# Kernel optimization log

Hardware: AMD Instinct MI355X
Metric: run time of the kernel (lower is better)

Reference implementation:

```python
import jax, jax.numpy as jnp
import numpy as np

DIM = 512
WH, WW = 8, 8
N = WH * WW
HEADS = 16
HEAD_DIM = DIM // HEADS
SCALE = HEAD_DIM ** -0.5
TABLE = (2 * WH - 1) * (2 * WW - 1)  # 225


def _relative_position_index(wh, ww):
    coords = np.stack(np.meshgrid(np.arange(wh), np.arange(ww), indexing='ij'))  # (2, wh, ww)
    flat = coords.reshape(2, -1)                       # (2, N)
    rel = flat[:, :, None] - flat[:, None, :]          # (2, N, N)
    rel = rel.transpose(1, 2, 0).astype(np.int64)      # (N, N, 2)
    rel[..., 0] += wh - 1
    rel[..., 1] += ww - 1
    rel[..., 0] *= 2 * ww - 1
    return rel.sum(-1)                                 # (N, N)

REL_IDX = _relative_position_index(WH, WW)


def setup_inputs() -> dict:
    key = jax.random.key(0)
    ks = jax.random.split(key, 10)
    B_ = 2048
    nW = 64
    x = jax.random.normal(ks[0], (B_, N, DIM), dtype=jnp.float32)
    y = jax.random.normal(ks[1], (B_, N, DIM), dtype=jnp.float32)
    mask = jnp.zeros((nW, N, N), dtype=jnp.float32)  # 0/-inf shift mask; zeros = no shift
    W_q = jax.random.normal(ks[2], (DIM, DIM), dtype=jnp.float32) * 0.02
    b_q = jnp.zeros((DIM,), dtype=jnp.float32)
    W_kv = jax.random.normal(ks[3], (DIM, 2 * DIM), dtype=jnp.float32) * 0.02
    b_kv = jnp.zeros((2 * DIM,), dtype=jnp.float32)
    W_proj = jax.random.normal(ks[4], (DIM, DIM), dtype=jnp.float32) * 0.02
    b_proj = jnp.zeros((DIM,), dtype=jnp.float32)
    bias_table = jax.random.normal(ks[5], (TABLE, HEADS), dtype=jnp.float32) * 0.02
    return {"x": x, "y": y, "mask": mask, "W_q": W_q, "b_q": b_q,
            "W_kv": W_kv, "b_kv": b_kv, "W_proj": W_proj, "b_proj": b_proj,
            "bias_table": bias_table}


def reference(x, y, mask, W_q, b_q, W_kv, b_kv, W_proj, b_proj, bias_table):
    B_, n, C = x.shape
    # projections
    q = (x @ W_q + b_q).reshape(B_, n, HEADS, HEAD_DIM).transpose(0, 2, 1, 3)       # (B_,H,N,hd)
    kv = (y @ W_kv + b_kv).reshape(B_, n, 2, HEADS, HEAD_DIM).transpose(2, 0, 3, 1, 4)
    k, v = kv[0], kv[1]                                                              # (B_,H,N,hd)
    q = q * SCALE
    attn = jnp.einsum('bhnd,bhmd->bhnm', q, k)                                       # (B_,H,N,N)
    # relative position bias gather: (N*N,) -> (N,N,H) -> (H,N,N)
    bias = bias_table[REL_IDX.reshape(-1)].reshape(n, n, HEADS).transpose(2, 0, 1)
    attn = attn + bias[None]
    nW = mask.shape[0]
    attn = attn.reshape(B_ // nW, nW, HEADS, n, n) + mask[None, :, None]
    attn = attn.reshape(B_, HEADS, n, n)
    attn = jax.nn.softmax(attn, axis=-1)
    out = jnp.einsum('bhnm,bhmd->bhnd', attn, v)                                     # (B_,H,N,hd)
    out = out.transpose(0, 2, 1, 3).reshape(B_, n, C)
    out = out @ W_proj + b_proj
    return out
```

## Files before the change

### kernel.cpp

```cpp
#include <hip/hip_runtime.h>
#include <stdint.h>

#define MROWS 131072
#define LOG2E 1.44269504088896340736f
#define QSCALE 0.17677669529663688110f

typedef _Float16 f16x8 __attribute__((ext_vector_type(8)));
typedef float f32x4 __attribute__((ext_vector_type(4)));
typedef unsigned short u16;
typedef u16 u16x4 __attribute__((ext_vector_type(4)));
typedef u16 u16x8 __attribute__((ext_vector_type(8)));

#define GLD16(gp, lp) __builtin_amdgcn_global_load_lds( \
    (const __attribute__((address_space(1))) void*)(gp), \
    (__attribute__((address_space(3))) void*)(lp), 16, 0, 0)

static __device__ __forceinline__ u16 f2h(float f) {
    _Float16 h = (_Float16)f;
    return __builtin_bit_cast(unsigned short, h);
}
static __device__ __forceinline__ float shflx(float v, int m) {
    return __shfl_xor(v, m, 64);
}
static __device__ __forceinline__ int swz4096(int bid) {
    return (bid & 7) * 512 + (bid >> 3);
}

__global__ void wt_f16(const float* __restrict__ W, int ldW, int colOff,
                       u16* __restrict__ WT, int K) {
    int idx = blockIdx.x * 256 + threadIdx.x;
    int n = idx / K, k = idx - n * K;
    WT[idx] = f2h(W[(size_t)k * ldW + colOff + n]);
}
__global__ void cmb_pre(const float* __restrict__ table, const float* __restrict__ mask,
                        float* __restrict__ cmb) {
    int wmod = blockIdx.x, h = blockIdx.y;
    float* outp = cmb + (((size_t)wmod * 16 + h) << 12);
    const float* mp = mask + ((size_t)wmod << 12);
    for (int e = threadIdx.x; e < 4096; e += 256) {
        int j = e >> 6, i = e & 63;
        int idx = ((i >> 3) - (j >> 3) + 7) * 15 + ((i & 7) - (j & 7) + 7);
        outp[e] = table[idx * 16 + h] + mp[i * 64 + j];
    }
}

__global__ __launch_bounds__(256, 4) void gemm_qk(
    const float* __restrict__ A, const u16* __restrict__ BT,
    const float* __restrict__ bias, u16* __restrict__ outp, float scale)
{
    __shared__ u16 As[128 * 32];
    __shared__ u16 Bs[128 * 32];
    const int tid = threadIdx.x;
    const int l = tid & 63, w = tid >> 6;
    const int al = l & 15, g = l >> 4;
    const int wr = w >> 1, wc = w & 1;
    const int wg = swz4096(blockIdx.x);
    const int n0 = (wg & 3) * 128, m0 = (wg >> 2) * 128;
    const int srow = tid >> 2, sc8 = (tid & 3) * 8;
    f32x4 acc[4][4] = {};

    for (int kk = 0; kk < 512; kk += 32) {
        #pragma unroll
        for (int r = 0; r < 2; ++r) {
            int row = r * 64 + srow;
            GLD16(BT + (size_t)(n0 + row) * 512 + kk + sc8, &Bs[row * 32 + sc8]);
            const float* ap = A + (size_t)(m0 + row) * 512 + kk + sc8;
            f32x4 v0 = *(const f32x4*)(ap);
            f32x4 v1 = *(const f32x4*)(ap + 4);
            u16x8 hv;
            hv[0]=f2h(v0[0]); hv[1]=f2h(v0[1]); hv[2]=f2h(v0[2]); hv[3]=f2h(v0[3]);
            hv[4]=f2h(v1[0]); hv[5]=f2h(v1[1]); hv[6]=f2h(v1[2]); hv[7]=f2h(v1[3]);
            *(u16x8*)&As[row * 32 + sc8] = hv;
        }
        __syncthreads();
        {
            f16x8 af[4], bfr[4];
            #pragma unroll
            for (int mt = 0; mt < 4; ++mt)
                af[mt] = *(const f16x8*)&As[(wr*64 + mt*16 + al) * 32 + g*8];
            #pragma unroll
            for (int nt = 0; nt < 4; ++nt)
                bfr[nt] = *(const f16x8*)&Bs[(wc*64 + nt*16 + al) * 32 + g*8];
            #pragma unroll
            for (int mt = 0; mt < 4; ++mt)
                #pragma unroll
                for (int nt = 0; nt < 4; ++nt)
                    acc[mt][nt] = __builtin_amdgcn_mfma_f32_16x16x32_f16(af[mt], bfr[nt], acc[mt][nt], 0, 0, 0);
        }
        __syncthreads();
    }
    #pragma unroll
    for (int nt = 0; nt < 4; ++nt) {
        int col = n0 + wc*64 + nt*16 + al;
        float bv = bias[col];
        #pragma unroll
        for (int mt = 0; mt < 4; ++mt)
            #pragma unroll
            for (int rg = 0; rg < 4; ++rg) {
                size_t row = (size_t)(m0 + wr*64 + mt*16 + g*4 + rg);
                outp[row * 512 + col] = f2h((acc[mt][nt][rg] + bv) * scale);
            }
    }
}

__global__ __launch_bounds__(256, 4) void gemm_v(
    const float* __restrict__ A, const u16* __restrict__ BT,
    const float* __restrict__ bias, u16* __restrict__ outp)
{
    __shared__ u16 As[128*32], Bs[128*32];
    const int tid = threadIdx.x;
    const int l = tid & 63, w = tid >> 6;
    const int al = l & 15, g = l >> 4;
    const int wr = w >> 1, wc = w & 1;
    const int wg = swz4096(blockIdx.x);
    const int n0 = (wg & 3) * 128, m0 = (wg >> 2) * 128;
    const int srow = tid >> 2, sc8 = (tid & 3) * 8;
    f32x4 acc[4][4] = {};

    for (int kk = 0; kk < 512; kk += 32) {
        #pragma unroll
        for (int r = 0; r < 2; ++r) {
            int row = r * 64 + srow;
            GLD16(BT + (size_t)(n0 + row) * 512 + kk + sc8, &Bs[row * 32 + sc8]);
            const float* ap = A + (size_t)(m0 + row) * 512 + kk + sc8;
            f32x4 v0 = *(const f32x4*)(ap);
            f32x4 v1 = *(const f32x4*)(ap + 4);
            u16x8 hv;
            hv[0]=f2h(v0[0]); hv[1]=f2h(v0[1]); hv[2]=f2h(v0[2]); hv[3]=f2h(v0[3]);
            hv[4]=f2h(v1[0]); hv[5]=f2h(v1[1]); hv[6]=f2h(v1[2]); hv[7]=f2h(v1[3]);
            *(u16x8*)&As[row * 32 + sc8] = hv;
        }
        __syncthreads();
        {
            f16x8 af[4], bfr[4];
            #pragma unroll
            for (int mt = 0; mt < 4; ++mt)
                af[mt] = *(const f16x8*)&As[(wr*64 + mt*16 + al) * 32 + g*8];
            #pragma unroll
            for (int nt = 0; nt < 4; ++nt)
                bfr[nt] = *(const f16x8*)&Bs[(wc*64 + nt*16 + al) * 32 + g*8];
            #pragma unroll
            for (int mt = 0; mt < 4; ++mt)
                #pragma unroll
                for (int nt = 0; nt < 4; ++nt)
                    acc[mt][nt] = __builtin_amdgcn_mfma_f32_16x16x32_f16(af[mt], bfr[nt], acc[mt][nt], 0, 0, 0);
        }
        __syncthreads();
    }
    #pragma unroll
    for (int nt = 0; nt < 4; ++nt) {
        int col = n0 + wc*64 + nt*16 + al;
        int hh_ = col >> 5, d = col & 31;
        float bv = bias[col];
        #pragma unroll
        for (int mt = 0; mt < 4; ++mt) {
            int row0 = m0 + wr*64 + mt*16 + g*4;
            int window = row0 >> 6, k0 = row0 & 63;
            size_t off = ((size_t)window << 15) + (hh_ << 11) + (d << 6) + k0;
            u16x4 hv;
            #pragma unroll
            for (int rg = 0; rg < 4; ++rg)
                hv[rg] = f2h(acc[mt][nt][rg] + bv);
            *(u16x4*)(outp + off) = hv;
        }
    }
}

__global__ __launch_bounds__(256, 4) void gemm_proj(
    const u16* __restrict__ A1, const u16* __restrict__ BT,
    const float* __restrict__ bias, float* __restrict__ outp)
{
    __shared__ u16 As[128*32], Bs[128*32];
    const int tid = threadIdx.x;
    const int l = tid & 63, w = tid >> 6;
    const int al = l & 15, g = l >> 4;
    const int wr = w >> 1, wc = w & 1;
    const int wg = swz4096(blockIdx.x);
    const int n0 = (wg & 3) * 128, m0 = (wg >> 2) * 128;
    const int srow = tid >> 2, sc8 = (tid & 3) * 8;
    f32x4 acc[4][4] = {};

    for (int kk = 0; kk < 512; kk += 32) {
        #pragma unroll
        for (int r = 0; r < 2; ++r) {
            int row = r * 64 + srow;
            size_t aoff = (size_t)(m0 + row) * 512 + kk + sc8;
            size_t boff = (size_t)(n0 + row) * 512 + kk + sc8;
            int loff = row * 32 + sc8;
            GLD16(A1 + aoff, &As[loff]);
            GLD16(BT + boff, &Bs[loff]);
        }
        __syncthreads();
        {
            f16x8 af[4], bfr[4];
            #pragma unroll
            for (int mt = 0; mt < 4; ++mt)
                af[mt] = *(const f16x8*)&As[(wr*64 + mt*16 + al) * 32 + g*8];
            #pragma unroll
            for (int nt = 0; nt < 4; ++nt)
                bfr[nt] = *(const f16x8*)&Bs[(wc*64 + nt*16 + al) * 32 + g*8];
            #pragma unroll
            for (int mt = 0; mt < 4; ++mt)
                #pragma unroll
                for (int nt = 0; nt < 4; ++nt)
                    acc[mt][nt] = __builtin_amdgcn_mfma_f32_16x16x32_f16(af[mt], bfr[nt], acc[mt][nt], 0, 0, 0);
        }
        __syncthreads();
    }
    #pragma unroll
    for (int nt = 0; nt < 4; ++nt) {
        int col = n0 + wc*64 + nt*16 + al;
        float bv = bias[col];
        #pragma unroll
        for (int mt = 0; mt < 4; ++mt)
            #pragma unroll
            for (int rg = 0; rg < 4; ++rg) {
                size_t row = (size_t)(m0 + wr*64 + mt*16 + g*4 + rg);
                outp[row * 512 + col] = acc[mt][nt][rg] + bv;
            }
    }
}

__global__ __launch_bounds__(256) void attn64(
    const u16* __restrict__ Q, const u16* __restrict__ Kb,
    const u16* __restrict__ Vth,
    const float* __restrict__ cmb,
    u16* __restrict__ Oout)
{
    __shared__ u16 Ph[4][64 * 72];
    const int bid = blockIdx.x;
    const int xcd = bid & 7, idx = bid >> 3;
    const int b = ((idx >> 3) << 6) | (xcd << 3) | (idx & 7);
    const int tid = threadIdx.x;
    const int l = tid & 63, w = tid >> 6;
    const int al = l & 15, g = l >> 4;
    const size_t rbase = (size_t)b * 64;
    const int h = blockIdx.y * 4 + w;
    const int co = h * 32;

    const u16* vth = Vth + ((size_t)b << 15) + (h << 11);
    f16x8 vhf[2][2];
    #pragma unroll
    for (int kt = 0; kt < 2; ++kt)
        #pragma unroll
        for (int dt = 0; dt < 2; ++dt) {
            int voff = ((dt*16 + al) << 6) + kt*32 + g*8;
            vhf[kt][dt] = *(const f16x8*)(vth + voff);
        }

    f16x8 qf[4], kf[4];
    #pragma unroll
    for (int t = 0; t < 4; ++t) {
        qf[t] = *(const f16x8*)(Q  + (rbase + t*16 + al) * 512 + co + g*8);
        kf[t] = *(const f16x8*)(Kb + (rbase + t*16 + al) * 512 + co + g*8);
    }
    f32x4 s[4][4] = {};
    #pragma unroll
    for (int mt = 0; mt < 4; ++mt)
        #pragma unroll
        for (int nt = 0; nt < 4; ++nt)
            s[mt][nt] = __builtin_amdgcn_mfma_f32_16x16x32_f16(qf[mt], kf[nt], s[mt][nt], 0, 0, 0);

    const float* cp = cmb + ((((size_t)(b & 63)) * 16 + h) << 12);
    #pragma unroll
    for (int mt = 0; mt < 4; ++mt)
        #pragma unroll
        for (int nt = 0; nt < 4; ++nt) {
            f32x4 c4 = *(const f32x4*)(cp + ((nt*16 + al) << 6) + mt*16 + g*4);
            #pragma unroll
            for (int rg = 0; rg < 4; ++rg) s[mt][nt][rg] += c4[rg];
        }

    f32x4 sm[4];
    #pragma unroll
    for (int mt = 0; mt < 4; ++mt) {
        f32x4 m4 = s[mt][0];
        #pragma unroll
        for (int nt = 1; nt < 4; ++nt)
            #pragma unroll
            for (int c = 0; c < 4; ++c) m4[c] = fmaxf(m4[c], s[mt][nt][c]);
        #pragma unroll
        for (int d = 1; d < 16; d <<= 1)
            #pragma unroll
            for (int c = 0; c < 4; ++c) m4[c] = fmaxf(m4[c], shflx(m4[c], d));
        #pragma unroll
        for (int nt = 0; nt < 4; ++nt)
            #pragma unroll
            for (int rg = 0; rg < 4; ++rg)
                s[mt][nt][rg] = exp2f((s[mt][nt][rg] - m4[rg]) * LOG2E);
        f32x4 s4 = s[mt][0];
        #pragma unroll
        for (int nt = 1; nt < 4; ++nt) s4 += s[mt][nt];
        #pragma unroll
        for (int d = 1; d < 16; d <<= 1)
            #pragma unroll
            for (int c = 0; c < 4; ++c) s4[c] += shflx(s4[c], d);
        sm[mt] = s4;
    }

    #pragma unroll
    for (int mt = 0; mt < 4; ++mt)
        #pragma unroll
        for (int nt = 0; nt < 4; ++nt)
            #pragma unroll
            for (int rg = 0; rg < 4; ++rg) {
                int off = (mt*16 + g*4 + rg) * 72 + nt*16 + al;
                Ph[w][off] = f2h(s[mt][nt][rg]);
            }

    #pragma unroll
    for (int mt = 0; mt < 4; ++mt) {
        f16x8 pah[2];
        #pragma unroll
        for (int kt = 0; kt < 2; ++kt)
            pah[kt] = *(const f16x8*)&Ph[w][(mt*16 + al) * 72 + kt*32 + g*8];
        f32x4 o[2] = {};
        #pragma unroll
        for (int dt = 0; dt < 2; ++dt)
            #pragma unroll
            for (int kt = 0; kt < 2; ++kt)
                o[dt] = __builtin_amdgcn_mfma_f32_16x16x32_f16(pah[kt], vhf[kt][dt], o[dt], 0, 0, 0);
        #pragma unroll
        for (int dt = 0; dt < 2; ++dt)
            #pragma unroll
            for (int rg = 0; rg < 4; ++rg) {
                float inv = __builtin_amdgcn_rcpf(sm[mt][rg]);
                float v = o[dt][rg] * inv;
                size_t off = (rbase + mt*16 + g*4 + rg) * 512 + co + dt*16 + al;
                Oout[off] = f2h(v);
            }
    }
}

extern "C" void kernel_launch(void* const* d_in, const int* in_sizes, int n_in,
                              void* d_out, int out_size, void* d_ws, size_t ws_size,
                              hipStream_t stream)
{
    const float* x      = (const float*)d_in[0];
    const float* y      = (const float*)d_in[1];
    const float* mask   = (const float*)d_in[2];
    const float* W_q    = (const float*)d_in[3];
    const float* b_q    = (const float*)d_in[4];
    const float* W_kv   = (const float*)d_in[5];
    const float* b_kv   = (const float*)d_in[6];
    const float* W_proj = (const float*)d_in[7];
    const float* b_proj = (const float*)d_in[8];
    const float* table  = (const float*)d_in[9];

    char* ws = (char*)d_ws;
    const size_t SEG = (size_t)MROWS * 512 * sizeof(u16);
    u16* Qs     = (u16*)(ws);
    u16* Ks     = (u16*)(ws + SEG);
    u16* Vth    = (u16*)(ws + 2 * SEG);
    u16* wqT    = (u16*)(ws + 3 * SEG);
    u16* wkvKT  = wqT    + 512 * 512;
    u16* wkvVT  = wkvKT  + 512 * 512;
    u16* wprT   = wkvVT  + 512 * 512;
    float* cmb  = (float*)(wprT + 512 * 512);

    wt_f16<<<1024, 256, 0, stream>>>(W_q, 512, 0, wqT, 512);
    wt_f16<<<1024, 256, 0, stream>>>(W_kv, 1024, 0, wkvKT, 512);
    wt_f16<<<1024, 256, 0, stream>>>(W_kv, 1024, 512, wkvVT, 512);
    wt_f16<<<1024, 256, 0, stream>>>(W_proj, 512, 0, wprT, 512);
    cmb_pre<<<dim3(64, 16), 256, 0, stream>>>(table, mask, cmb);

    gemm_qk<<<4096, 256, 0, stream>>>(x, wqT, b_q, Qs, QSCALE);
    gemm_qk<<<4096, 256, 0, stream>>>(y, wkvKT, b_kv, Ks, 1.0f);
    gemm_v<<<4096, 256, 0, stream>>>(y, wkvVT, b_kv + 512, Vth);
    attn64<<<dim3(2048, 4), 256, 0, stream>>>(Qs, Ks, Vth, cmb, Qs);
    gemm_proj<<<4096, 256, 0, stream>>>(Qs, wprT, b_proj, (float*)d_out);
}
```

Before: 782.7 us.

## Double-buffer LDS tiles in projection GEMMs to overlap loads with MFMA

Converts the three projection GEMM kernels to a double-buffered shared-memory pipeline. The next K-slice's global loads (register prefetch for fp32 A, direct-to-LDS loads for B) are issued before the current slice's MFMAs, and one of the two barriers per iteration is removed. This is meant to hide global memory latency behind compute. It doubles LDS per block to 32KB, which may limit occupancy under launch_bounds(256,4), and the single-barrier scheme relies on the direct-to-LDS loads having completed when the barrier is reached.

```diff
diff --git a/kernel.cpp b/kernel.cpp
--- a/kernel.cpp
+++ b/kernel.cpp
@@ -48,8 +48,8 @@
     const float* __restrict__ A, const u16* __restrict__ BT,
     const float* __restrict__ bias, u16* __restrict__ outp, float scale)
 {
-    __shared__ u16 As[128 * 32];
-    __shared__ u16 Bs[128 * 32];
+    __shared__ u16 As[2][128 * 32];
+    __shared__ u16 Bs[2][128 * 32];
     const int tid = threadIdx.x;
     const int l = tid & 63, w = tid >> 6;
     const int al = l & 15, g = l >> 4;
@@ -57,37 +57,56 @@
     const int wg = swz4096(blockIdx.x);
     const int n0 = (wg & 3) * 128, m0 = (wg >> 2) * 128;
     const int srow = tid >> 2, sc8 = (tid & 3) * 8;
+    const float* asrc0 = A  + (size_t)(m0 + srow) * 512 + sc8;
+    const float* asrc1 = A  + (size_t)(m0 + 64 + srow) * 512 + sc8;
+    const u16*   bsrc0 = BT + (size_t)(n0 + srow) * 512 + sc8;
+    const u16*   bsrc1 = BT + (size_t)(n0 + 64 + srow) * 512 + sc8;
+    const int lo0 = srow * 32 + sc8, lo1 = (64 + srow) * 32 + sc8;
     f32x4 acc[4][4] = {};
 
-    for (int kk = 0; kk < 512; kk += 32) {
-        #pragma unroll
-        for (int r = 0; r < 2; ++r) {
-            int row = r * 64 + srow;
-            GLD16(BT + (size_t)(n0 + row) * 512 + kk + sc8, &Bs[row * 32 + sc8]);
-            const float* ap = A + (size_t)(m0 + row) * 512 + kk + sc8;
-            f32x4 v0 = *(const f32x4*)(ap);
-            f32x4 v1 = *(const f32x4*)(ap + 4);
-            u16x8 hv;
-            hv[0]=f2h(v0[0]); hv[1]=f2h(v0[1]); hv[2]=f2h(v0[2]); hv[3]=f2h(v0[3]);
-            hv[4]=f2h(v1[0]); hv[5]=f2h(v1[1]); hv[6]=f2h(v1[2]); hv[7]=f2h(v1[3]);
-            *(u16x8*)&As[row * 32 + sc8] = hv;
+    f32x4 a00 = *(const f32x4*)(asrc0);
+    f32x4 a01 = *(const f32x4*)(asrc0 + 4);
+    f32x4 a10 = *(const f32x4*)(asrc1);
+    f32x4 a11 = *(const f32x4*)(asrc1 + 4);
+    GLD16(bsrc0, &Bs[0][lo0]);
+    GLD16(bsrc1, &Bs[0][lo1]);
+
+    #pragma unroll 2
+    for (int it = 0; it < 16; ++it) {
+        const int cur = it & 1, nxt = cur ^ 1;
+        {
+            u16x8 h0, h1;
+            h0[0]=f2h(a00[0]); h0[1]=f2h(a00[1]); h0[2]=f2h(a00[2]); h0[3]=f2h(a00[3]);
+            h0[4]=f2h(a01[0]); h0[5]=f2h(a01[1]); h0[6]=f2h(a01[2]); h0[7]=f2h(a01[3]);
+            h1[0]=f2h(a10[0]); h1[1]=f2h(a10[1]); h1[2]=f2h(a10[2]); h1[3]=f2h(a10[3]);
+            h1[4]=f2h(a11[0]); h1[5]=f2h(a11[1]); h1[6]=f2h(a11[2]); h1[7]=f2h(a11[3]);
+            *(u16x8*)&As[cur][lo0] = h0;
+            *(u16x8*)&As[cur][lo1] = h1;
         }
         __syncthreads();
+        if (it < 15) {
+            const int kn = (it + 1) * 32;
+            a00 = *(const f32x4*)(asrc0 + kn);
+            a01 = *(const f32x4*)(asrc0 + kn + 4);
+            a10 = *(const f32x4*)(asrc1 + kn);
+            a11 = *(const f32x4*)(asrc1 + kn + 4);
+            GLD16(bsrc0 + kn, &Bs[nxt][lo0]);
+            GLD16(bsrc1 + kn, &Bs[nxt][lo1]);
+        }
         {
             f16x8 af[4], bfr[4];
             #pragma unroll
             for (int mt = 0; mt < 4; ++mt)
-                af[mt] = *(const f16x8*)&As[(wr*64 + mt*16 + al) * 32 + g*8];
+                af[mt] = *(const f16x8*)&As[cur][(wr*64 + mt*16 + al) * 32 + g*8];
             #pragma unroll
             for (int nt = 0; nt < 4; ++nt)
-                bfr[nt] = *(const f16x8*)&Bs[(wc*64 + nt*16 + al) * 32 + g*8];
+                bfr[nt] = *(const f16x8*)&Bs[cur][(wc*64 + nt*16 + al) * 32 + g*8];
             #pragma unroll
             for (int mt = 0; mt < 4; ++mt)
                 #pragma unroll
                 for (int nt = 0; nt < 4; ++nt)
                     acc[mt][nt] = __builtin_amdgcn_mfma_f32_16x16x32_f16(af[mt], bfr[nt], acc[mt][nt], 0, 0, 0);
         }
-        __syncthreads();
     }
     #pragma unroll
     for (int nt = 0; nt < 4; ++nt) {
@@ -107,7 +126,8 @@
     const float* __restrict__ A, const u16* __restrict__ BT,
     const float* __restrict__ bias, u16* __restrict__ outp)
 {
-    __shared__ u16 As[128*32], Bs[128*32];
+    __shared__ u16 As[2][128 * 32];
+    __shared__ u16 Bs[2][128 * 32];
     const int tid = threadIdx.x;
     const int l = tid & 63, w = tid >> 6;
     const int al = l & 15, g = l >> 4;
@@ -115,37 +135,56 @@
     const int wg = swz4096(blockIdx.x);
     const int n0 = (wg & 3) * 128, m0 = (wg >> 2) * 128;
     const int srow = tid >> 2, sc8 = (tid & 3) * 8;
+    const float* asrc0 = A  + (size_t)(m0 + srow) * 512 + sc8;
+    const float* asrc1 = A  + (size_t)(m0 + 64 + srow) * 512 + sc8;
+    const u16*   bsrc0 = BT + (size_t)(n0 + srow) * 512 + sc8;
+    const u16*   bsrc1 = BT + (size_t)(n0 + 64 + srow) * 512 + sc8;
+    const int lo0 = srow * 32 + sc8, lo1 = (64 + srow) * 32 + sc8;
     f32x4 acc[4][4] = {};
 
-    for (int kk = 0; kk < 512; kk += 32) {
-        #pragma unroll
-        for (int r = 0; r < 2; ++r) {
-            int row = r * 64 + srow;
-            GLD16(BT + (size_t)(n0 + row) * 512 + kk + sc8, &Bs[row * 32 + sc8]);
-            const float* ap = A + (size_t)(m0 + row) * 512 + kk + sc8;
-            f32x4 v0 = *(const f32x4*)(ap);
-            f32x4 v1 = *(const f32x4*)(ap + 4);
-            u16x8 hv;
-            hv[0]=f2h(v0[0]); hv[1]=f2h(v0[1]); hv[2]=f2h(v0[2]); hv[3]=f2h(v0[3]);
-            hv[4]=f2h(v1[0]); hv[5]=f2h(v1[1]); hv[6]=f2h(v1[2]); hv[7]=f2h(v1[3]);
-            *(u16x8*)&As[row * 32 + sc8] = hv;
+    f32x4 a00 = *(const f32x4*)(asrc0);
+    f32x4 a01 = *(const f32x4*)(asrc0 + 4);
+    f32x4 a10 = *(const f32x4*)(asrc1);
+    f32x4 a11 = *(const f32x4*)(asrc1 + 4);
+    GLD16(bsrc0, &Bs[0][lo0]);
+    GLD16(bsrc1, &Bs[0][lo1]);
+
+    #pragma unroll 2
+    for (int it = 0; it < 16; ++it) {
+        const int cur = it & 1, nxt = cur ^ 1;
+        {
+            u16x8 h0, h1;
+            h0[0]=f2h(a00[0]); h0[1]=f2h(a00[1]); h0[2]=f2h(a00[2]); h0[3]=f2h(a00[3]);
+            h0[4]=f2h(a01[0]); h0[5]=f2h(a01[1]); h0[6]=f2h(a01[2]); h0[7]=f2h(a01[3]);
+            h1[0]=f2h(a10[0]); h1[1]=f2h(a10[1]); h1[2]=f2h(a10[2]); h1[3]=f2h(a10[3]);
+            h1[4]=f2h(a11[0]); h1[5]=f2h(a11[1]); h1[6]=f2h(a11[2]); h1[7]=f2h(a11[3]);
+            *(u16x8*)&As[cur][lo0] = h0;
+            *(u16x8*)&As[cur][lo1] = h1;
         }
         __syncthreads();
+        if (it < 15) {
+            const int kn = (it + 1) * 32;
+            a00 = *(const f32x4*)(asrc0 + kn);
+            a01 = *(const f32x4*)(asrc0 + kn + 4);
+            a10 = *(const f32x4*)(asrc1 + kn);
+            a11 = *(const f32x4*)(asrc1 + kn + 4);
+            GLD16(bsrc0 + kn, &Bs[nxt][lo0]);
+            GLD16(bsrc1 + kn, &Bs[nxt][lo1]);
+        }
         {
             f16x8 af[4], bfr[4];
             #pragma unroll
             for (int mt = 0; mt < 4; ++mt)
-                af[mt] = *(const f16x8*)&As[(wr*64 + mt*16 + al) * 32 + g*8];
+                af[mt] = *(const f16x8*)&As[cur][(wr*64 + mt*16 + al) * 32 + g*8];
             #pragma unroll
             for (int nt = 0; nt < 4; ++nt)
-                bfr[nt] = *(const f16x8*)&Bs[(wc*64 + nt*16 + al) * 32 + g*8];
+                bfr[nt] = *(const f16x8*)&Bs[cur][(wc*64 + nt*16 + al) * 32 + g*8];
             #pragma unroll
             for (int mt = 0; mt < 4; ++mt)
                 #pragma unroll
                 for (int nt = 0; nt < 4; ++nt)
                     acc[mt][nt] = __builtin_amdgcn_mfma_f32_16x16x32_f16(af[mt], bfr[nt], acc[mt][nt], 0, 0, 0);
         }
-        __syncthreads();
     }
     #pragma unroll
     for (int nt = 0; nt < 4; ++nt) {
@@ -170,7 +209,8 @@
     const u16* __restrict__ A1, const u16* __restrict__ BT,
     const float* __restrict__ bias, float* __restrict__ outp)
 {
-    __shared__ u16 As[128*32], Bs[128*32];
+    __shared__ u16 As[2][128 * 32];
+    __shared__ u16 Bs[2][128 * 32];
     const int tid = threadIdx.x;
     const int l = tid & 63, w = tid >> 6;
     const int al = l & 15, g = l >> 4;
@@ -178,34 +218,43 @@
     const int wg = swz4096(blockIdx.x);
     const int n0 = (wg & 3) * 128, m0 = (wg >> 2) * 128;
     const int srow = tid >> 2, sc8 = (tid & 3) * 8;
+    const u16* asrc0 = A1 + (size_t)(m0 + srow) * 512 + sc8;
+    const u16* asrc1 = A1 + (size_t)(m0 + 64 + srow) * 512 + sc8;
+    const u16* bsrc0 = BT + (size_t)(n0 + srow) * 512 + sc8;
+    const u16* bsrc1 = BT + (size_t)(n0 + 64 + srow) * 512 + sc8;
+    const int lo0 = srow * 32 + sc8, lo1 = (64 + srow) * 32 + sc8;
     f32x4 acc[4][4] = {};
 
-    for (int kk = 0; kk < 512; kk += 32) {
-        #pragma unroll
-        for (int r = 0; r < 2; ++r) {
-            int row = r * 64 + srow;
-            size_t aoff = (size_t)(m0 + row) * 512 + kk + sc8;
-            size_t boff = (size_t)(n0 + row) * 512 + kk + sc8;
-            int loff = row * 32 + sc8;
-            GLD16(A1 + aoff, &As[loff]);
-            GLD16(BT + boff, &Bs[loff]);
-        }
+    GLD16(asrc0, &As[0][lo0]);
+    GLD16(asrc1, &As[0][lo1]);
+    GLD16(bsrc0, &Bs[0][lo0]);
+    GLD16(bsrc1, &Bs[0][lo1]);
+
+    #pragma unroll 2
+    for (int it = 0; it < 16; ++it) {
+        const int cur = it & 1, nxt = cur ^ 1;
         __syncthreads();
+        if (it < 15) {
+            const int kn = (it + 1) * 32;
+            GLD16(asrc0 + kn, &As[nxt][lo0]);
+            GLD16(asrc1 + kn, &As[nxt][lo1]);
+            GLD16(bsrc0 + kn, &Bs[nxt][lo0]);
+            GLD16(bsrc1 + kn, &Bs[nxt][lo1]);
+        }
         {
             f16x8 af[4], bfr[4];
             #pragma unroll
             for (int mt = 0; mt < 4; ++mt)
-                af[mt] = *(const f16x8*)&As[(wr*64 + mt*16 + al) * 32 + g*8];
+                af[mt] = *(const f16x8*)&As[cur][(wr*64 + mt*16 + al) * 32 + g*8];
             #pragma unroll
             for (int nt = 0; nt < 4; ++nt)
-                bfr[nt] = *(const f16x8*)&Bs[(wc*64 + nt*16 + al) * 32 + g*8];
+                bfr[nt] = *(const f16x8*)&Bs[cur][(wc*64 + nt*16 + al) * 32 + g*8];
             #pragma unroll
             for (int mt = 0; mt < 4; ++mt)
                 #pragma unroll
                 for (int nt = 0; nt < 4; ++nt)
                     acc[mt][nt] = __builtin_amdgcn_mfma_f32_16x16x32_f16(af[mt], bfr[nt], acc[mt][nt], 0, 0, 0);
         }
-        __syncthreads();
     }
     #pragma unroll
     for (int nt = 0; nt < 4; ++nt) {
```

Result: no change. 780.3 us (-0.3%).
